# Optimization experiments

Measured on AMD Instinct MI355X. Metric: run time of the kernel, lower is better.

Reference implementation:

```python
import jax, jax.numpy as jnp
import numpy as np

N, D, H, E, K, C = 8192, 1024, 2048, 8, 2, 2560  # tokens, d_model, hidden, experts, top_k, capacity


def setup_inputs() -> dict:
    key = jax.random.key(0)
    ks = jax.random.split(key, 8)
    s_in, s_h = 1.0 / np.sqrt(D), 1.0 / np.sqrt(H)
    return {
        "x": jax.random.normal(ks[0], (N, D), jnp.float32),
        "Wg": jax.random.uniform(ks[1], (D, E), jnp.float32, -s_in, s_in),
        "bg": jnp.zeros((E,), jnp.float32),
        "W1": jax.random.uniform(ks[2], (E, D, H), jnp.float32, -s_in, s_in),
        "b1": jnp.zeros((E, H), jnp.float32),
        "W2": jax.random.uniform(ks[3], (E, H, H), jnp.float32, -s_h, s_h),
        "b2": jnp.zeros((E, H), jnp.float32),
    }


def reference(x, Wg, bg, W1, b1, W2, b2):
    n = x.shape[0]
    logits = x @ Wg + bg                                  # [N, E]
    probs = jax.nn.softmax(logits, axis=-1)
    topk_probs, topk_idx = jax.lax.top_k(probs, K)        # [N, K]

    # auxiliary losses (training mode)
    importance = probs.sum(0)
    importance_loss = jnp.var(importance) / (E ** 2)
    rows = jnp.arange(n)[:, None]
    mask = jnp.zeros_like(probs).at[rows, topk_idx].set(1.0)
    routing_probs = probs * mask
    expert_usage = mask.mean(0)
    routing_weights = routing_probs.mean(0)
    load_balance_loss = E * (expert_usage * routing_weights).sum()
    aux_loss = importance_loss + load_balance_loss

    # dispatch: rank of each (token, k) slot within its expert, in flat order
    flat_e = topk_idx.reshape(-1)                          # [N*K]
    flat_p = topk_probs.reshape(-1)                        # [N*K]
    sample_idx = jnp.repeat(jnp.arange(n), K)              # [N*K]
    oh = (flat_e[:, None] == jnp.arange(E)[None, :]).astype(jnp.int32)  # [N*K, E]
    rank = jnp.take_along_axis(jnp.cumsum(oh, axis=0), flat_e[:, None], axis=1)[:, 0] - 1
    keep = rank < C                                        # capacity truncation (first-come)
    r_safe = jnp.where(keep, rank, C)                      # C is out-of-bounds -> dropped

    buf = jnp.zeros((E, C, D), x.dtype).at[flat_e, r_safe].set(x[sample_idx], mode="drop")
    h = jax.nn.gelu(jnp.einsum("ecd,edh->ech", buf, W1) + b1[:, None, :], approximate=False)
    y = jnp.einsum("ech,eho->eco", h, W2) + b2[:, None, :]  # [E, C, H]

    gathered = y[flat_e, jnp.minimum(r_safe, C - 1)]       # [N*K, H]
    weighted = gathered * (flat_p * keep.astype(x.dtype))[:, None]
    outputs = jnp.zeros((n, H), x.dtype).at[sample_idx].add(weighted)
    return outputs, aux_loss
```

## Files before the change

kernel.cpp:

```cpp
#include <hip/hip_runtime.h>
#include <math.h>
#include <stdint.h>

#define N_TOK 8192
#define DMODEL 1024
#define HID 2048
#define NEXP 8
#define TOPK 2
#define CAP 2560
#define NT1 640
#define NTALL 1280

typedef __bf16 bf16x8 __attribute__((ext_vector_type(8)));
typedef float f32x4 __attribute__((ext_vector_type(4)));
typedef unsigned int u32x4 __attribute__((ext_vector_type(4)));

__device__ __forceinline__ unsigned short f2b(float f) {
    unsigned int u = __builtin_bit_cast(unsigned int, f);
    u += 0x7fffu + ((u >> 16) & 1u);
    return (unsigned short)(u >> 16);
}
__device__ __forceinline__ float b2f(unsigned short s) {
    unsigned int u = ((unsigned int)s) << 16;
    return __builtin_bit_cast(float, u);
}

__device__ __forceinline__ float gelu_f(float v) {
    const float ax = fabsf(v) * 0.70710678118654752440f;
    const float t = __builtin_amdgcn_rcpf(1.f + 0.3275911f * ax);
    float poly = ((((1.061405429f * t - 1.453152027f) * t + 1.421413741f) * t
                   - 0.284496736f) * t + 0.254829592f) * t;
    float er = 1.f - poly * __expf(-ax * ax);
    er = (v >= 0.f) ? er : -er;
    return 0.5f * v * (1.f + er);
}

__device__ __forceinline__ void gload_lds16(const void* g, void* lds) {
    __builtin_amdgcn_global_load_lds(
        (const __attribute__((address_space(1))) unsigned int*)(uintptr_t)g,
        (__attribute__((address_space(3))) unsigned int*)(unsigned int)(uintptr_t)lds,
        16, 0, 0);
}

__global__ __launch_bounds__(256) void gate_kernel(
    const float* __restrict__ x, const float* __restrict__ Wg,
    const float* __restrict__ bg,
    int* __restrict__ flat_e, float* __restrict__ flat_p,
    float* __restrict__ imp_part, float* __restrict__ sel_part,
    unsigned short* __restrict__ xbf)
{
    __shared__ float s_imp[4][NEXP];
    __shared__ float s_sel[4][NEXP];
    const int wave = threadIdx.x >> 6;
    const int lane = threadIdx.x & 63;
    const int t = blockIdx.x * 4 + wave;

    float acc[NEXP];
#pragma unroll
    for (int e = 0; e < NEXP; ++e) acc[e] = 0.f;
    const float* xr = x + (size_t)t * DMODEL;
    unsigned short* xbr = xbf + (size_t)t * DMODEL;
    for (int d = lane; d < DMODEL; d += 64) {
        const float xv = xr[d];
        xbr[d] = f2b(xv);
#pragma unroll
        for (int e = 0; e < NEXP; ++e) acc[e] += xv * Wg[d * NEXP + e];
    }
#pragma unroll
    for (int off = 32; off > 0; off >>= 1) {
#pragma unroll
        for (int e = 0; e < NEXP; ++e) acc[e] += __shfl_xor(acc[e], off);
    }
    float lg[NEXP], mx = -1e30f;
#pragma unroll
    for (int e = 0; e < NEXP; ++e) { lg[e] = acc[e] + bg[e]; mx = fmaxf(mx, lg[e]); }
    float p[NEXP], s = 0.f;
#pragma unroll
    for (int e = 0; e < NEXP; ++e) { p[e] = expf(lg[e] - mx); s += p[e]; }
    const float inv = 1.f / s;
#pragma unroll
    for (int e = 0; e < NEXP; ++e) p[e] *= inv;

    int i0 = 0;
#pragma unroll
    for (int e = 1; e < NEXP; ++e) if (p[e] > p[i0]) i0 = e;
    int i1 = (i0 == 0) ? 1 : 0;
#pragma unroll
    for (int e = 0; e < NEXP; ++e) if (e != i0 && p[e] > p[i1]) i1 = e;

    if (lane == 0) {
        flat_e[2 * t] = i0;  flat_e[2 * t + 1] = i1;
        flat_p[2 * t] = p[i0]; flat_p[2 * t + 1] = p[i1];
#pragma unroll
        for (int e = 0; e < NEXP; ++e) {
            s_imp[wave][e] = p[e];
            s_sel[wave][e] = (e == i0) ? p[i0] : ((e == i1) ? p[i1] : 0.f);
        }
    }
    __syncthreads();
    if (threadIdx.x < NEXP) {
        const int e = threadIdx.x;
        float a = 0.f, b = 0.f;
#pragma unroll
        for (int w = 0; w < 4; ++w) { a += s_imp[w][e]; b += s_sel[w][e]; }
        imp_part[blockIdx.x * NEXP + e] = a;
        sel_part[blockIdx.x * NEXP + e] = b;
    }
}

__global__ __launch_bounds__(1024) void scan_kernel(
    const int* __restrict__ flat_e, int* __restrict__ slot_rank,
    int* __restrict__ row_token, int* __restrict__ n_kept,
    int* __restrict__ cnt_full, unsigned short* __restrict__ xbf_pad,
    int* __restrict__ ctrs)
{
    __shared__ int wave_tot[16][NEXP];
    __shared__ int base[NEXP];
    const int tid = threadIdx.x, lane = tid & 63, w = tid >> 6;
    if (tid < NEXP) base[tid] = 0;
    if (tid < 81) ctrs[tid] = 0;
    for (int i = tid; i < DMODEL; i += 1024) xbf_pad[i] = 0;
    __syncthreads();
    const unsigned long long ltmask =
        (lane == 0) ? 0ull : (~0ull >> (64 - lane));
    for (int chunk = 0; chunk < (N_TOK * TOPK) / 1024; ++chunk) {
        const int s = chunk * 1024 + tid;
        const int e = flat_e[s];
        int prefix = 0;
#pragma unroll
        for (int ee = 0; ee < NEXP; ++ee) {
            unsigned long long m = __ballot(e == ee);
            if (ee == e) prefix = __popcll(m & ltmask);
            if (lane == 0) wave_tot[w][ee] = __popcll(m);
        }
        __syncthreads();
        int before = base[e];
        for (int ww = 0; ww < w; ++ww) before += wave_tot[ww][e];
        const int rank = before + prefix;
        slot_rank[s] = rank;
        if (rank < CAP) row_token[e * CAP + rank] = s >> 1;
        __syncthreads();
        if (tid < NEXP) {
            int add = 0;
#pragma unroll
            for (int ww = 0; ww < 16; ++ww) add += wave_tot[ww][tid];
            base[tid] += add;
        }
        __syncthreads();
    }
    for (int i = tid; i < NEXP * CAP; i += 1024) {
        const int ee = i / CAP;
        const int r = i - ee * CAP;
        const int ne = base[ee] < CAP ? base[ee] : CAP;
        if (r >= ne) row_token[i] = N_TOK;
    }
    if (tid < NEXP) {
        n_kept[tid] = min(base[tid], CAP);
        cnt_full[tid] = base[tid];
    }
}

__global__ __launch_bounds__(256) void transpose_cvt(
    const float* __restrict__ W, unsigned short* __restrict__ Wt,
    const int R, const int Cdim)
{
    __shared__ unsigned short s[64][66];
    const int e = blockIdx.z;
    const int c0 = blockIdx.x * 64, r0 = blockIdx.y * 64;
    const float* We = W + (size_t)e * R * Cdim;
    unsigned short* Wte = Wt + (size_t)e * R * Cdim;
    const int tid = threadIdx.x;
    const int lr = tid >> 6;
    const int lc = tid & 63;
#pragma unroll
    for (int i = 0; i < 16; ++i)
        s[lr + i * 4][lc] =
            f2b(__builtin_nontemporal_load(&We[(size_t)(r0 + lr + i * 4) * Cdim + c0 + lc]));
    __syncthreads();
#pragma unroll
    for (int pass = 0; pass < 2; ++pass) {
        const int cc = (tid >> 3) + pass * 32;
        const int rq = (tid & 7) * 8;
        unsigned short v[8];
#pragma unroll
        for (int k = 0; k < 8; ++k) v[k] = s[rq + k][cc];
        u32x4 o;
        o[0] = v[0] | ((unsigned)v[1] << 16); o[1] = v[2] | ((unsigned)v[3] << 16);
        o[2] = v[4] | ((unsigned)v[5] << 16); o[3] = v[6] | ((unsigned)v[7] << 16);
        *(u32x4*)&Wte[(size_t)(c0 + cc) * R + r0 + rq] = o;
    }
}

#define VMGATE4() do { asm volatile("s_waitcnt vmcnt(4)" ::: "memory"); \
                       __builtin_amdgcn_sched_barrier(0); } while (0)
#define VMGATE0() do { asm volatile("s_waitcnt vmcnt(0)" ::: "memory"); \
                       __builtin_amdgcn_sched_barrier(0); } while (0)
#define NOGATE() ((void)0)

#define PHASE(mf0, STAGE_STMT, TAIL_STMT) do {                                   \
    bf16x8 a0 = lda(c, (mf0), 0), a1 = lda(c, (mf0), 1);                         \
    bf16x8 a2 = lda(c, (mf0) + 1, 0), a3 = lda(c, (mf0) + 1, 1);                 \
    STAGE_STMT;                                                                  \
    __builtin_amdgcn_s_barrier();                                                \
    asm volatile("s_waitcnt lgkmcnt(0)" ::: "memory");                           \
    __builtin_amdgcn_sched_barrier(0);                                           \
    __builtin_amdgcn_s_setprio(1);                                               \
    _Pragma("unroll")                                                            \
    for (int nf = 0; nf < 4; ++nf) {                                             \
        acc[(mf0)][nf] = __builtin_amdgcn_mfma_f32_16x16x32_bf16(                \
            a0, bfr[nf][0], acc[(mf0)][nf], 0, 0, 0);                            \
        acc[(mf0)][nf] = __builtin_amdgcn_mfma_f32_16x16x32_bf16(                \
            a1, bfr[nf][1], acc[(mf0)][nf], 0, 0, 0);                            \
        acc[(mf0) + 1][nf] = __builtin_amdgcn_mfma_f32_16x16x32_bf16(            \
            a2, bfr[nf][0], acc[(mf0) + 1][nf], 0, 0, 0);                        \
        acc[(mf0) + 1][nf] = __builtin_amdgcn_mfma_f32_16x16x32_bf16(            \
            a3, bfr[nf][1], acc[(mf0) + 1][nf], 0, 0, 0);                        \
    }                                                                            \
    __builtin_amdgcn_s_setprio(0);                                               \
    TAIL_STMT;                                                                   \
    __builtin_amdgcn_s_barrier();                                                \
} while (0)

__global__ __launch_bounds__(512, 1) void mfma_gemm_fused(
    const unsigned short* __restrict__ xbf,
    const unsigned short* __restrict__ w1t,
    const unsigned short* __restrict__ w2t,
    const float* __restrict__ b1, const float* __restrict__ b2,
    unsigned short* __restrict__ hbuf,
    unsigned short* __restrict__ ybuf,
    const int* __restrict__ row_token, const int* __restrict__ n_kept,
    int* __restrict__ ctr)
{
    __shared__ unsigned short smem[81920];
    int* s_item = (int*)((char*)smem + 163836);
    int* done = ctr + 1;

    const int t = threadIdx.x;
    const int w = t >> 6, lane = t & 63;
    const int wm = w >> 2, wn = w & 3;
    const int l15 = lane & 15, lq = lane >> 4;
    const int srow_lo = t >> 3;

    const int sx = (l15 & 4) << 3;
    const int kbx0 = (lq * 16) ^ sx;
    const int kbx1 = (64 + lq * 16) ^ sx;
    auto lda = [&](int cbuf, int mf, int ks) -> bf16x8 {
        return *(const bf16x8*)((const char*)smem + cbuf * 32768 +
                                (wm * 128 + mf * 16 + l15) * 128 + (ks ? kbx1 : kbx0));
    };
    auto ldb = [&](int cbuf, int nf, int ks) -> bf16x8 {
        return *(const bf16x8*)((const char*)smem + 65536 + cbuf * 32768 +
                                (wn * 64 + nf * 16 + l15) * 128 + (ks ? kbx1 : kbx0));
    };

    for (;;) {
        __syncthreads();
        if (t == 0) *s_item = atomicAdd(ctr, 1);
        __syncthreads();
        const int item = *s_item;
        if (item >= NTALL) break;

        const bool g2 = item >= NT1;
        const int it = g2 ? item - NT1 : item;
        const int e = it / 80;
        const int rem = it - e * 80;
        const int m = rem % 10;
        const int n = rem / 10;
        const int m0 = m * 256, n0 = n * 256;
        if (m0 >= n_kept[e]) continue;

        if (g2) {
            if (t == 0) {
                while (__hip_atomic_load(&done[e * 10 + m], __ATOMIC_ACQUIRE,
                                         __HIP_MEMORY_SCOPE_AGENT) < 8)
                    __builtin_amdgcn_s_sleep(8);
            }
            __syncthreads();
        }

        const int Kdim = g2 ? HID : DMODEL;
        const int NT = Kdim >> 6;
        const unsigned short* A  = g2 ? hbuf : xbf;
        const unsigned short* Wt = g2 ? w2t : w1t;

        long abase[2][2], bbase[2][2];
#pragma unroll
        for (int h = 0; h < 2; ++h) {
#pragma unroll
            for (int cc = 0; cc < 2; ++cc) {
                const int srow = h * 128 + cc * 64 + srow_lo;
                const int skoff = ((t & 7) * 8) ^ ((srow & 4) << 2);
                long ar;
                if (g2) ar = ((long)e * CAP + m0 + srow) * (long)Kdim;
                else    ar = (long)row_token[e * CAP + m0 + srow] * Kdim;
                abase[h][cc] = ar + skoff;
                bbase[h][cc] = ((long)e * HID + n0 + srow) * (long)Kdim + skoff;
            }
        }
        auto stageA = [&](int buf, int h0, int ktile) {
            const long ko = (long)ktile * 64;
            char* base = (char*)smem + buf * 32768 + h0 * 16384 + w * 1024;
            gload_lds16(A + (h0 ? abase[1][0] : abase[0][0]) + ko, base);
            gload_lds16(A + (h0 ? abase[1][1] : abase[0][1]) + ko, base + 8192);
        };
        auto stageB = [&](int buf, int h0, int ktile) {
            const long ko = (long)ktile * 64;
            char* base = (char*)smem + 65536 + buf * 32768 + h0 * 16384 + w * 1024;
            gload_lds16(Wt + (h0 ? bbase[1][0] : bbase[0][0]) + ko, base);
            gload_lds16(Wt + (h0 ? bbase[1][1] : bbase[0][1]) + ko, base + 8192);
        };

        f32x4 acc[8][4];
#pragma unroll
        for (int mm = 0; mm < 8; ++mm)
#pragma unroll
            for (int nn = 0; nn < 4; ++nn) acc[mm][nn] = (f32x4)0.f;

        stageA(0, 0, 0); stageA(0, 1, 0);
        stageB(0, 0, 0); stageB(0, 1, 0);
        stageB(1, 0, 1); stageB(1, 1, 1);
        VMGATE4();
        __builtin_amdgcn_s_barrier();

        int bcur = 0;
        for (int kt = 0; kt < NT; ++kt) {
            const int c = kt & 1, o = c ^ 1;
            const int ktA = kt + 1;
            const int ktB = kt + 2;
            int bst = bcur + 2; if (bst >= 3) bst -= 3;

            bf16x8 bfr[4][2];
#pragma unroll
            for (int nf = 0; nf < 4; ++nf) {
                bfr[nf][0] = ldb(bcur, nf, 0);
                bfr[nf][1] = ldb(bcur, nf, 1);
            }
            PHASE(0, if (ktA < NT) stageA(o, 0, ktA), NOGATE());
            PHASE(2, if (ktA < NT) stageA(o, 1, ktA), NOGATE());
            PHASE(4, if (ktB < NT) stageB(bst, 0, ktB), NOGATE());
            if (ktB < NT) {
                PHASE(6, stageB(bst, 1, ktB), VMGATE4());
            } else {
                PHASE(6, NOGATE(), VMGATE0());
            }
            bcur = (bcur == 2) ? 0 : bcur + 1;
        }

        const float* be = (g2 ? b2 : b1) + (size_t)e * HID;
        unsigned short* outp = g2 ? ybuf : hbuf;
        float bv[4];
#pragma unroll
        for (int nf = 0; nf < 4; ++nf)
            bv[nf] = be[n0 + wn * 64 + nf * 16 + l15];
#pragma unroll
        for (int mf = 0; mf < 8; ++mf) {
#pragma unroll
            for (int j = 0; j < 4; ++j) {
                const int row = m0 + wm * 128 + mf * 16 + lq * 4 + j;
                unsigned short* orow =
                    outp + ((size_t)e * CAP + row) * HID + n0 + wn * 64 + l15;
#pragma unroll
                for (int nf = 0; nf < 4; ++nf) {
                    float v = acc[mf][nf][j] + bv[nf];
                    if (!g2) v = gelu_f(v);
                    orow[nf * 16] = f2b(v);
                }
            }
        }

        if (!g2) {
            __syncthreads();
            if (t == 0)
                __hip_atomic_fetch_add(&done[e * 10 + m], 1, __ATOMIC_RELEASE,
                                       __HIP_MEMORY_SCOPE_AGENT);
        }
    }
}

__global__ __launch_bounds__(256) void combine_kernel(
    const unsigned short* __restrict__ y, const int* __restrict__ flat_e,
    const float* __restrict__ flat_p, const int* __restrict__ slot_rank,
    float* __restrict__ out)
{
    const int t = blockIdx.x;
    const int e0 = flat_e[2 * t], e1 = flat_e[2 * t + 1];
    const int r0 = slot_rank[2 * t], r1 = slot_rank[2 * t + 1];
    const bool k0 = r0 < CAP, k1 = r1 < CAP;
    const float w0 = k0 ? flat_p[2 * t] : 0.f;
    const float w1 = k1 ? flat_p[2 * t + 1] : 0.f;
    const unsigned short* y0 = y + ((size_t)e0 * CAP + (k0 ? r0 : 0)) * HID;
    const unsigned short* y1 = y + ((size_t)e1 * CAP + (k1 ? r1 : 0)) * HID;
    float* orow = out + (size_t)t * HID;
    const int c = threadIdx.x * 8;
    u32x4 av = k0 ? __builtin_nontemporal_load((const u32x4*)(y0 + c)) : (u32x4)0u;
    u32x4 bv = k1 ? __builtin_nontemporal_load((const u32x4*)(y1 + c)) : (u32x4)0u;
    float o[8];
    auto comb2 = [&](unsigned int a, unsigned int b, float* dst) {
        dst[0] = w0 * b2f((unsigned short)(a & 0xffffu)) +
                 w1 * b2f((unsigned short)(b & 0xffffu));
        dst[1] = w0 * b2f((unsigned short)(a >> 16)) +
                 w1 * b2f((unsigned short)(b >> 16));
    };
    comb2(av[0], bv[0], o + 0); comb2(av[1], bv[1], o + 2);
    comb2(av[2], bv[2], o + 4); comb2(av[3], bv[3], o + 6);
    f32x4 o0 = {o[0], o[1], o[2], o[3]};
    f32x4 o1 = {o[4], o[5], o[6], o[7]};
    __builtin_nontemporal_store(o0, (f32x4*)(orow + c));
    __builtin_nontemporal_store(o1, (f32x4*)(orow + c + 4));
}

__global__ __launch_bounds__(64) void aux_kernel(
    const float* __restrict__ imp_part, const float* __restrict__ sel_part,
    const int* __restrict__ cnt_full, float* __restrict__ out_aux,
    const int nparts)
{
    const int lane = threadIdx.x;
    __shared__ float imp_s[NEXP], sel_s[NEXP];
    for (int e = 0; e < NEXP; ++e) {
        float a = 0.f, b = 0.f;
        for (int i = lane; i < nparts; i += 64) {
            a += imp_part[i * NEXP + e];
            b += sel_part[i * NEXP + e];
        }
#pragma unroll
        for (int off = 32; off > 0; off >>= 1) {
            a += __shfl_xor(a, off);
            b += __shfl_xor(b, off);
        }
        if (lane == 0) { imp_s[e] = a; sel_s[e] = b; }
    }
    __syncthreads();
    if (lane == 0) {
        double mean = 0.0;
        for (int e = 0; e < NEXP; ++e) mean += imp_s[e];
        mean /= NEXP;
        double var = 0.0;
        for (int e = 0; e < NEXP; ++e) {
            const double d = (double)imp_s[e] - mean;
            var += d * d;
        }
        var /= NEXP;
        double load = 0.0;
        for (int e = 0; e < NEXP; ++e)
            load += ((double)cnt_full[e] / N_TOK) * ((double)sel_s[e] / N_TOK);
        load *= NEXP;
        out_aux[0] = (float)(var / (NEXP * NEXP) + load);
    }
}

extern "C" void kernel_launch(void* const* d_in, const int* in_sizes, int n_in,
                              void* d_out, int out_size, void* d_ws, size_t ws_size,
                              hipStream_t stream) {
    const float* x  = (const float*)d_in[0];
    const float* Wg = (const float*)d_in[1];
    const float* bg = (const float*)d_in[2];
    const float* W1 = (const float*)d_in[3];
    const float* b1 = (const float*)d_in[4];
    const float* W2 = (const float*)d_in[5];
    const float* b2 = (const float*)d_in[6];
    float* out = (float*)d_out;
    (void)in_sizes; (void)n_in; (void)out_size; (void)ws_size;

    char* ws = (char*)d_ws;
    size_t off = 0;
    auto alloc = [&](size_t bytes) -> void* {
        void* p = ws + off;
        off = (off + bytes + 255) & ~(size_t)255;
        return p;
    };
    int*   n_kept    = (int*)alloc(NEXP * sizeof(int));
    int*   cnt_full  = (int*)alloc(NEXP * sizeof(int));
    int*   ctrs      = (int*)alloc(81 * sizeof(int));
    int*   flat_e    = (int*)alloc((size_t)N_TOK * TOPK * sizeof(int));
    float* flat_p    = (float*)alloc((size_t)N_TOK * TOPK * sizeof(float));
    int*   slot_rank = (int*)alloc((size_t)N_TOK * TOPK * sizeof(int));
    int*   row_tok   = (int*)alloc((size_t)NEXP * CAP * sizeof(int));
    float* imp_part  = (float*)alloc((size_t)(N_TOK / 4) * NEXP * sizeof(float));
    float* sel_part  = (float*)alloc((size_t)(N_TOK / 4) * NEXP * sizeof(float));
    unsigned short* xbf  = (unsigned short*)alloc((size_t)(N_TOK + 1) * DMODEL * 2);
    unsigned short* w1t  = (unsigned short*)alloc((size_t)NEXP * DMODEL * HID * 2);
    unsigned short* w2t  = (unsigned short*)alloc((size_t)NEXP * HID * HID * 2);
    unsigned short* hbuf = (unsigned short*)alloc((size_t)NEXP * CAP * HID * 2);
    unsigned short* ybuf = (unsigned short*)alloc((size_t)NEXP * CAP * HID * 2);

    gate_kernel<<<N_TOK / 4, 256, 0, stream>>>(x, Wg, bg, flat_e, flat_p,
                                               imp_part, sel_part, xbf);
    scan_kernel<<<1, 1024, 0, stream>>>(flat_e, slot_rank, row_tok, n_kept,
                                        cnt_full, xbf + (size_t)N_TOK * DMODEL,
                                        ctrs);

    transpose_cvt<<<dim3(HID / 64, DMODEL / 64, NEXP), 256, 0, stream>>>(W1, w1t, DMODEL, HID);
    transpose_cvt<<<dim3(HID / 64, HID / 64, NEXP), 256, 0, stream>>>(W2, w2t, HID, HID);

    mfma_gemm_fused<<<256, 512, 0, stream>>>(xbf, w1t, w2t, b1, b2, hbuf, ybuf,
                                             row_tok, n_kept, ctrs);

    combine_kernel<<<N_TOK, 256, 0, stream>>>(ybuf, flat_e, flat_p, slot_rank, out);
    aux_kernel<<<1, 64, 0, stream>>>(imp_part, sel_part, cnt_full,
                                     out + (size_t)N_TOK * HID, N_TOK / 4);
}
```

Before: 449.2 us.

## Fuse weight transpose-convert into persistent GEMM kernel with per-slice readiness flags

Removes the two standalone transpose_cvt launches and folds W1/W2 fp32-to-bf16 transposition into the persistent MFMA work queue as extra work items. Items are interleaved so W1 slices come first, then some GEMM1 tiles, then W2 slices. GEMM tiles spin on per-(expert,n-slice) flags before consuming the transposed weights. This overlaps weight conversion with GEMM work and drops launch gaps, at the cost of spin-waiting and transposition done by 512-thread blocks with lower parallelism. The GEMM2 output store also becomes nontemporal.

New measurement: 526.7 us. 17.2% more time.

```diff
diff --git a/kernel.cpp b/kernel.cpp
--- a/kernel.cpp
+++ b/kernel.cpp
@@ -8,8 +8,7 @@
 #define NEXP 8
 #define TOPK 2
 #define CAP 2560
-#define NT1 640
-#define NTALL 1280
+#define NTALL 1408
 
 typedef __bf16 bf16x8 __attribute__((ext_vector_type(8)));
 typedef float f32x4 __attribute__((ext_vector_type(4)));
@@ -118,7 +117,7 @@
     __shared__ int base[NEXP];
     const int tid = threadIdx.x, lane = tid & 63, w = tid >> 6;
     if (tid < NEXP) base[tid] = 0;
-    if (tid < 81) ctrs[tid] = 0;
+    if (tid < 209) ctrs[tid] = 0;
     for (int i = tid; i < DMODEL; i += 1024) xbf_pad[i] = 0;
     __syncthreads();
     const unsigned long long ltmask =
@@ -157,37 +156,6 @@
     if (tid < NEXP) {
         n_kept[tid] = min(base[tid], CAP);
         cnt_full[tid] = base[tid];
-    }
-}
-
-__global__ __launch_bounds__(256) void transpose_cvt(
-    const float* __restrict__ W, unsigned short* __restrict__ Wt,
-    const int R, const int Cdim)
-{
-    __shared__ unsigned short s[64][66];
-    const int e = blockIdx.z;
-    const int c0 = blockIdx.x * 64, r0 = blockIdx.y * 64;
-    const float* We = W + (size_t)e * R * Cdim;
-    unsigned short* Wte = Wt + (size_t)e * R * Cdim;
-    const int tid = threadIdx.x;
-    const int lr = tid >> 6;
-    const int lc = tid & 63;
-#pragma unroll
-    for (int i = 0; i < 16; ++i)
-        s[lr + i * 4][lc] =
-            f2b(__builtin_nontemporal_load(&We[(size_t)(r0 + lr + i * 4) * Cdim + c0 + lc]));
-    __syncthreads();
-#pragma unroll
-    for (int pass = 0; pass < 2; ++pass) {
-        const int cc = (tid >> 3) + pass * 32;
-        const int rq = (tid & 7) * 8;
-        unsigned short v[8];
-#pragma unroll
-        for (int k = 0; k < 8; ++k) v[k] = s[rq + k][cc];
-        u32x4 o;
-        o[0] = v[0] | ((unsigned)v[1] << 16); o[1] = v[2] | ((unsigned)v[3] << 16);
-        o[2] = v[4] | ((unsigned)v[5] << 16); o[3] = v[6] | ((unsigned)v[7] << 16);
-        *(u32x4*)&Wte[(size_t)(c0 + cc) * R + r0 + rq] = o;
     }
 }
 
@@ -221,19 +189,23 @@
     __builtin_amdgcn_s_barrier();                                                \
 } while (0)
 
-__global__ __launch_bounds__(512, 1) void mfma_gemm_fused(
+__global__ __launch_bounds__(512, 1) void mfma_fused(
     const unsigned short* __restrict__ xbf,
-    const unsigned short* __restrict__ w1t,
-    const unsigned short* __restrict__ w2t,
+    const float* __restrict__ W1,
+    const float* __restrict__ W2,
+    unsigned short* w1t,
+    unsigned short* w2t,
     const float* __restrict__ b1, const float* __restrict__ b2,
-    unsigned short* __restrict__ hbuf,
+    unsigned short* hbuf,
     unsigned short* __restrict__ ybuf,
     const int* __restrict__ row_token, const int* __restrict__ n_kept,
     int* __restrict__ ctr)
 {
     __shared__ unsigned short smem[81920];
     int* s_item = (int*)((char*)smem + 163836);
-    int* done = ctr + 1;
+    int* hdone  = ctr + 1;
+    int* w1flag = ctr + 81;
+    int* w2flag = ctr + 145;
 
     const int t = threadIdx.x;
     const int w = t >> 6, lane = t & 63;
@@ -260,23 +232,69 @@
         const int item = *s_item;
         if (item >= NTALL) break;
 
-        const bool g2 = item >= NT1;
-        const int it = g2 ? item - NT1 : item;
-        const int e = it / 80;
-        const int rem = it - e * 80;
+        bool isT = false, isW2 = false;
+        int tIdx = 0, gIdx = 0;
+        bool g2 = false;
+        if (item < 64)        { isT = true; isW2 = false; tIdx = item; }
+        else if (item < 128)  { gIdx = item - 64;  g2 = false; }
+        else if (item < 192)  { isT = true; isW2 = true; tIdx = item - 128; }
+        else if (item < 768)  { gIdx = item - 128; g2 = false; }
+        else                  { gIdx = item - 768; g2 = true; }
+
+        if (isT) {
+            const int e = tIdx >> 3, n = tIdx & 7;
+            const int R = isW2 ? HID : DMODEL;
+            const float* Wsrc = (isW2 ? W2 : W1) + (size_t)e * R * HID + n * 256;
+            unsigned short* Wdst =
+                (isW2 ? w2t : w1t) + ((size_t)e * HID + n * 256) * R;
+            unsigned short (*ts)[66] = (unsigned short(*)[66])smem;
+            const int lr = t >> 6, lc = t & 63;
+            const int cc = t >> 3, rq = (t & 7) * 8;
+            for (int kb = 0; kb < R; kb += 64) {
+                for (int nb = 0; nb < 4; ++nb) {
+                    __syncthreads();
+#pragma unroll
+                    for (int i = 0; i < 8; ++i)
+                        ts[lr + i * 8][lc] = f2b(__builtin_nontemporal_load(
+                            &Wsrc[(size_t)(kb + lr + i * 8) * HID + nb * 64 + lc]));
+                    __syncthreads();
+                    unsigned short v[8];
+#pragma unroll
+                    for (int k2 = 0; k2 < 8; ++k2) v[k2] = ts[rq + k2][cc];
+                    u32x4 o;
+                    o[0] = v[0] | ((unsigned)v[1] << 16);
+                    o[1] = v[2] | ((unsigned)v[3] << 16);
+                    o[2] = v[4] | ((unsigned)v[5] << 16);
+                    o[3] = v[6] | ((unsigned)v[7] << 16);
+                    *(u32x4*)&Wdst[(size_t)(nb * 64 + cc) * R + kb + rq] = o;
+                }
+            }
+            __syncthreads();
+            if (t == 0)
+                __hip_atomic_fetch_add(&(isW2 ? w2flag : w1flag)[tIdx], 1,
+                                       __ATOMIC_RELEASE, __HIP_MEMORY_SCOPE_AGENT);
+            continue;
+        }
+
+        const int e = gIdx / 80;
+        const int rem = gIdx - e * 80;
         const int m = rem % 10;
         const int n = rem / 10;
         const int m0 = m * 256, n0 = n * 256;
         if (m0 >= n_kept[e]) continue;
 
-        if (g2) {
-            if (t == 0) {
-                while (__hip_atomic_load(&done[e * 10 + m], __ATOMIC_ACQUIRE,
+        if (t == 0) {
+            int* wf = g2 ? &w2flag[e * 8 + n] : &w1flag[e * 8 + n];
+            while (__hip_atomic_load(wf, __ATOMIC_ACQUIRE,
+                                     __HIP_MEMORY_SCOPE_AGENT) < 1)
+                __builtin_amdgcn_s_sleep(8);
+            if (g2) {
+                while (__hip_atomic_load(&hdone[e * 10 + m], __ATOMIC_ACQUIRE,
                                          __HIP_MEMORY_SCOPE_AGENT) < 8)
                     __builtin_amdgcn_s_sleep(8);
             }
-            __syncthreads();
-        }
+        }
+        __syncthreads();
 
         const int Kdim = g2 ? HID : DMODEL;
         const int NT = Kdim >> 6;
@@ -287,14 +305,14 @@
 #pragma unroll
         for (int h = 0; h < 2; ++h) {
 #pragma unroll
-            for (int cc = 0; cc < 2; ++cc) {
-                const int srow = h * 128 + cc * 64 + srow_lo;
+            for (int cc2 = 0; cc2 < 2; ++cc2) {
+                const int srow = h * 128 + cc2 * 64 + srow_lo;
                 const int skoff = ((t & 7) * 8) ^ ((srow & 4) << 2);
                 long ar;
                 if (g2) ar = ((long)e * CAP + m0 + srow) * (long)Kdim;
                 else    ar = (long)row_token[e * CAP + m0 + srow] * Kdim;
-                abase[h][cc] = ar + skoff;
-                bbase[h][cc] = ((long)e * HID + n0 + srow) * (long)Kdim + skoff;
+                abase[h][cc2] = ar + skoff;
+                bbase[h][cc2] = ((long)e * HID + n0 + srow) * (long)Kdim + skoff;
             }
         }
         auto stageA = [&](int buf, int h0, int ktile) {
@@ -362,8 +380,12 @@
 #pragma unroll
                 for (int nf = 0; nf < 4; ++nf) {
                     float v = acc[mf][nf][j] + bv[nf];
-                    if (!g2) v = gelu_f(v);
-                    orow[nf * 16] = f2b(v);
+                    if (!g2) {
+                        v = gelu_f(v);
+                        orow[nf * 16] = f2b(v);
+                    } else {
+                        __builtin_nontemporal_store(f2b(v), &orow[nf * 16]);
+                    }
                 }
             }
         }
@@ -371,7 +393,7 @@
         if (!g2) {
             __syncthreads();
             if (t == 0)
-                __hip_atomic_fetch_add(&done[e * 10 + m], 1, __ATOMIC_RELEASE,
+                __hip_atomic_fetch_add(&hdone[e * 10 + m], 1, __ATOMIC_RELEASE,
                                        __HIP_MEMORY_SCOPE_AGENT);
         }
     }
@@ -470,7 +492,7 @@
     };
     int*   n_kept    = (int*)alloc(NEXP * sizeof(int));
     int*   cnt_full  = (int*)alloc(NEXP * sizeof(int));
-    int*   ctrs      = (int*)alloc(81 * sizeof(int));
+    int*   ctrs      = (int*)alloc(209 * sizeof(int));
     int*   flat_e    = (int*)alloc((size_t)N_TOK * TOPK * sizeof(int));
     float* flat_p    = (float*)alloc((size_t)N_TOK * TOPK * sizeof(float));
     int*   slot_rank = (int*)alloc((size_t)N_TOK * TOPK * sizeof(int));
@@ -489,11 +511,8 @@
                                         cnt_full, xbf + (size_t)N_TOK * DMODEL,
                                         ctrs);
 
-    transpose_cvt<<<dim3(HID / 64, DMODEL / 64, NEXP), 256, 0, stream>>>(W1, w1t, DMODEL, HID);
-    transpose_cvt<<<dim3(HID / 64, HID / 64, NEXP), 256, 0, stream>>>(W2, w2t, HID, HID);
-
-    mfma_gemm_fused<<<256, 512, 0, stream>>>(xbf, w1t, w2t, b1, b2, hbuf, ybuf,
-                                             row_tok, n_kept, ctrs);
+    mfma_fused<<<256, 512, 0, stream>>>(xbf, W1, W2, w1t, w2t, b1, b2,
+                                        hbuf, ybuf, row_tok, n_kept, ctrs);
 
     combine_kernel<<<N_TOK, 256, 0, stream>>>(ybuf, flat_e, flat_p, slot_rank, out);
     aux_kernel<<<1, 64, 0, stream>>>(imp_part, sel_part, cnt_full,
```
